# Kernel optimization log

Hardware: AMD Instinct MI355X
Metric: run time of the kernel (lower is better)

## Reference

```python
import jax, jax.numpy as jnp
import numpy as np

B, C, H, Wd = 16, 512, 56, 56
WCH = 128  # W_ch: projection rank of phi/rou


def setup_inputs() -> dict:
    key = jax.random.key(0)
    ks = jax.random.split(key, 8)
    s = 0.02
    return {
        "x": jax.random.normal(ks[0], (B, C, H, Wd), dtype=jnp.float32),
        "y": jax.random.normal(ks[1], (B, C, H, Wd), dtype=jnp.float32),
        # phi: Conv2d(C, WCH, 1) -> weight [WCH, C], bias [WCH]
        "phi_w": jax.random.normal(ks[2], (WCH, C), dtype=jnp.float32) * s,
        "phi_b": jnp.zeros((WCH,), dtype=jnp.float32),
        # rou: Conv2d(C, WCH, 1) applied to globally pooled y -> acts as Linear
        "rou_w": jax.random.normal(ks[3], (WCH, C), dtype=jnp.float32) * s,
        "rou_b": jnp.zeros((WCH,), dtype=jnp.float32),
        # zeta: Linear(C, C)
        "zeta_w": jax.random.normal(ks[4], (C, C), dtype=jnp.float32) * s,
        "zeta_b": jnp.zeros((C,), dtype=jnp.float32),
    }


def reference(x, y, phi_w, phi_b, rou_w, rou_b, zeta_w, zeta_b):
    b, c, h, w = x.shape
    hw = h * w
    # phi_xT = relu(phi(x)).view(B, WCH, HW); phi_x = transpose -> [B, HW, WCH]
    phi_xT = jax.nn.relu(jnp.einsum('kc,bchw->bkhw', phi_w, x) + phi_b[None, :, None, None])
    phi_x = phi_xT.reshape(b, -1, hw).transpose(0, 2, 1)  # [B, HW, WCH]
    # rou_y = sigmoid(rou(global_avg_pool(y))) -> [B, WCH]
    pooled = y.mean(axis=(2, 3))  # [B, C]
    rou_y = jax.nn.sigmoid(pooled @ rou_w.T + rou_b)  # [B, WCH]
    # D_i = sum_j (phi_x diag(rou) phi_x^T)_{ij} = sum_k phi_x[i,k] rou[k] s[k]
    s = phi_x.sum(axis=1)  # [B, WCH], column sums
    D = jnp.einsum('bnk,bk,bk->bn', phi_x, rou_y, s)  # [B, HW]
    inv_sqrt = 1.0 / jnp.sqrt(D + 1e-8)
    P = phi_x * inv_sqrt[..., None]  # diag(D^-1/2) @ phi_x, [B, HW, WCH]
    # x.view(B, -1, C): raw row-major reshape of [B,C,H,W] (NOT a transpose)
    x_trans = x.reshape(b, hw, c)
    # LX = x_trans - P diag(rou) P^T x_trans, re-associated right-to-left
    t = jnp.einsum('bnk,bnc->bkc', P, x_trans)          # P^T x_trans, [B, WCH, C]
    LX = x_trans - jnp.einsum('bnk,bk,bkc->bnc', P, rou_y, t)
    # zeta Linear + dropout(eval: identity) + relu, residual add
    out = jax.nn.relu(LX @ zeta_w.T + zeta_b)
    return x + out.reshape(b, c, h, w)
```

## Files before the change

kernel.cpp:

```cpp
#include <hip/hip_runtime.h>
#include <math.h>

#define B_  16
#define C_  512
#define HW_ 3136
#define K_  128
#define CHW (C_ * HW_)

typedef __bf16 bf16x8_t __attribute__((ext_vector_type(8)));
typedef __bf16 bf16x4_t __attribute__((ext_vector_type(4)));
typedef __bf16 bf16x2_t __attribute__((ext_vector_type(2)));
typedef float floatx4  __attribute__((ext_vector_type(4)));

typedef const __attribute__((address_space(1))) void* gas_ptr;
typedef __attribute__((address_space(3))) void*       las_ptr;

static __device__ __forceinline__ unsigned short bfbits(__bf16 v) {
    return __builtin_bit_cast(unsigned short, v);
}

__device__ __forceinline__ void stage128x64(const __bf16* __restrict__ base, long ld,
                                            int row0, int rowmax, int k0,
                                            __bf16* lds, int t) {
    int w = t >> 6;
    #pragma unroll
    for (int i = 0; i < 4; ++i) {
        int u = i * 256 + t;
        int m = u >> 3, slot = u & 7;
        int kg = slot ^ (m & 7);
        int r = row0 + m; if (r > rowmax) r = rowmax;
        const __bf16* g = base + (long)r * ld + (k0 + kg * 8);
        __bf16* l = lds + (size_t)(i * 256 + w * 64) * 8;
        __builtin_amdgcn_global_load_lds((gas_ptr)g, (las_ptr)l, 16, 0, 0);
    }
}

__device__ __forceinline__ void stage_tr_phi(const __bf16* __restrict__ src,
                                             int n0, int p0, char* Bs, int t) {
    int ng = t & 15;
    int cp2 = (t >> 4) * 2;
    #pragma unroll
    for (int ci = 0; ci < 2; ++ci) {
        int cc = cp2 + ci * 32;
        const __bf16* g0 = src + (long)(p0 + cc) * HW_ + n0 + ng * 8;
        bf16x8_t v0 = *(const bf16x8_t*)g0;
        bf16x8_t v1 = *(const bf16x8_t*)(g0 + HW_);
        int r8 = cc >> 3, sub = (cc & 7) >> 1;
        #pragma unroll
        for (int j = 0; j < 8; ++j) {
            int row = ng * 8 + j;
            int slot = (r8 + row + (row >> 3)) & 7;
            unsigned int pr = ((unsigned int)bfbits(v1[j]) << 16) | bfbits(v0[j]);
            *(unsigned int*)(Bs + row * 144 + slot * 16 + sub * 4) = pr;
        }
    }
}

__device__ __forceinline__ void stage_tr_t(const __bf16* __restrict__ src,
                                           const float* __restrict__ isrc,
                                           int c0, int p0, char* Bs, int t) {
    int cg = t & 15;
    int np2 = (t >> 4) * 2;
    #pragma unroll
    for (int ni = 0; ni < 2; ++ni) {
        int nn = np2 + ni * 32;
        int n = p0 + nn;
        float s0 = isrc[n], s1 = isrc[n + 1];
        const __bf16* g0 = src + (long)n * C_ + c0 + cg * 8;
        bf16x8_t v0 = *(const bf16x8_t*)g0;
        bf16x8_t v1 = *(const bf16x8_t*)(g0 + C_);
        int r8 = nn >> 3, sub = (nn & 7) >> 1;
        #pragma unroll
        for (int j = 0; j < 8; ++j) {
            int row = cg * 8 + j;
            int slot = (r8 + row + (row >> 3)) & 7;
            __bf16 a0 = (__bf16)((float)v0[j] * s0);
            __bf16 a1 = (__bf16)((float)v1[j] * s1);
            unsigned int pr = ((unsigned int)bfbits(a1) << 16) | bfbits(a0);
            *(unsigned int*)(Bs + row * 144 + slot * 16 + sub * 4) = pr;
        }
    }
}

__device__ __forceinline__ void mma_step64(const char* As, const char* Bs,
                                           floatx4 acc[4][4], int aoff, int boff,
                                           int q, int lxor) {
    #pragma unroll
    for (int h = 0; h < 2; ++h) {
        int s = (((h * 4 + q) ^ lxor) << 4);
        bf16x8_t af[4], bf[4];
        #pragma unroll
        for (int i = 0; i < 4; ++i) af[i] = *(const bf16x8_t*)(As + aoff + i * 2048 + s);
        #pragma unroll
        for (int i = 0; i < 4; ++i) bf[i] = *(const bf16x8_t*)(Bs + boff + i * 2048 + s);
        #pragma unroll
        for (int mi = 0; mi < 4; ++mi)
            #pragma unroll
            for (int ni = 0; ni < 4; ++ni)
                acc[mi][ni] = __builtin_amdgcn_mfma_f32_16x16x32_bf16(af[mi], bf[ni], acc[mi][ni], 0, 0, 0);
    }
}

__device__ __forceinline__ void mma_step_mix(const char* As, const char* Bs,
                                             floatx4 acc[4][4], int lm, int q,
                                             int wrow, int wcol) {
    int lxor = lm & 7;
    int aoff = (wrow * 64 + lm) * 128;
    #pragma unroll
    for (int h = 0; h < 2; ++h) {
        int g = h * 4 + q;
        int sa = (g ^ lxor) << 4;
        bf16x8_t af[4], bf[4];
        #pragma unroll
        for (int i = 0; i < 4; ++i) af[i] = *(const bf16x8_t*)(As + aoff + i * 2048 + sa);
        #pragma unroll
        for (int i = 0; i < 4; ++i) {
            int brow = wcol * 64 + i * 16 + lm;
            int slot = (g + brow + (brow >> 3)) & 7;
            bf[i] = *(const bf16x8_t*)(Bs + brow * 144 + slot * 16);
        }
        #pragma unroll
        for (int mi = 0; mi < 4; ++mi)
            #pragma unroll
            for (int ni = 0; ni < 4; ++ni)
                acc[mi][ni] = __builtin_amdgcn_mfma_f32_16x16x32_bf16(af[mi], bf[ni], acc[mi][ni], 0, 0, 0);
    }
}


__global__ __launch_bounds__(256) void k_pool(const float* __restrict__ y,
                                              float* __restrict__ pooled) {
    int bc = blockIdx.x;
    const float* yp = y + (long)bc * HW_;
    int t = threadIdx.x;
    float acc = 0.f;
    #pragma unroll
    for (int i = 0; i < 4; ++i) {
        int n4 = t + i * 256;
        if (n4 < 784) {
            float4 v = *reinterpret_cast<const float4*>(yp + (long)n4 * 4);
            acc += v.x + v.y + v.z + v.w;
        }
    }
    #pragma unroll
    for (int off = 32; off > 0; off >>= 1) acc += __shfl_xor(acc, off, 64);
    __shared__ float red[4];
    if ((t & 63) == 0) red[t >> 6] = acc;
    __syncthreads();
    if (t == 0) pooled[bc] = (red[0] + red[1] + red[2] + red[3]) * (1.0f / HW_);
}

__global__ __launch_bounds__(64) void k_rou(const float* __restrict__ pooled,
                                            const float* __restrict__ rou_w,
                                            const float* __restrict__ rou_b,
                                            float* __restrict__ rou_y) {
    int k = blockIdx.x;
    int b = blockIdx.y;
    int lane = threadIdx.x;
    const float* pr = pooled + b * C_;
    const float* wr = rou_w + (long)k * C_;
    float acc = 0.f;
    #pragma unroll
    for (int i = 0; i < 2; ++i) {
        int c = (lane + i * 64) * 4;
        float4 w4 = *reinterpret_cast<const float4*>(wr + c);
        float4 p4 = *reinterpret_cast<const float4*>(pr + c);
        acc += w4.x * p4.x + w4.y * p4.y + w4.z * p4.z + w4.w * p4.w;
    }
    #pragma unroll
    for (int off = 32; off > 0; off >>= 1) acc += __shfl_xor(acc, off, 64);
    if (lane == 0) rou_y[b * K_ + k] = 1.0f / (1.0f + expf(-(acc + rou_b[k])));
}

__global__ __launch_bounds__(256) void k_cast8(const float* __restrict__ a,
                                               __bf16* __restrict__ o) {
    long i = ((long)blockIdx.x * 256 + threadIdx.x) * 8;
    float4 v0 = *reinterpret_cast<const float4*>(a + i);
    float4 v1 = *reinterpret_cast<const float4*>(a + i + 4);
    bf16x8_t r;
    r[0] = (__bf16)v0.x; r[1] = (__bf16)v0.y; r[2] = (__bf16)v0.z; r[3] = (__bf16)v0.w;
    r[4] = (__bf16)v1.x; r[5] = (__bf16)v1.y; r[6] = (__bf16)v1.z; r[7] = (__bf16)v1.w;
    *reinterpret_cast<bf16x8_t*>(o + i) = r;
}


__global__ __launch_bounds__(256) void k_phi_m(const __bf16* __restrict__ xbf2,
                                               const __bf16* __restrict__ pwbf,
                                               const float* __restrict__ phi_b,
                                               __bf16* __restrict__ phi_kn,
                                               __bf16* __restrict__ phi_nk,
                                               float* __restrict__ sbuf) {
    int b = blockIdx.y;
    int n0 = blockIdx.x * 128;
    __shared__ __attribute__((aligned(16))) char smem[2 * 34816];
    int t = threadIdx.x, w = t >> 6, lane = t & 63;
    int lm = lane & 15, q = lane >> 4;
    int wrow = w >> 1, wcol = w & 1;
    floatx4 acc[4][4];
    #pragma unroll
    for (int i = 0; i < 4; ++i)
        #pragma unroll
        for (int j = 0; j < 4; ++j) acc[i][j] = (floatx4){0.f, 0.f, 0.f, 0.f};

    const __bf16* Bb = xbf2 + (long)b * CHW;

    stage128x64(pwbf, C_, 0, K_ - 1, 0, (__bf16*)smem, t);
    stage_tr_phi(Bb, n0, 0, smem + 16384, t);
    __syncthreads();
    int cur = 0;
    #pragma unroll
    for (int s = 0; s < 8; ++s) {
        char* cb = smem + cur * 34816;
        if (s < 7) {
            char* nb = smem + (cur ^ 1) * 34816;
            int p0 = (s + 1) * 64;
            stage128x64(pwbf, C_, 0, K_ - 1, p0, (__bf16*)nb, t);
            stage_tr_phi(Bb, n0, p0, nb + 16384, t);
        }
        mma_step_mix(cb, cb + 16384, acc, lm, q, wrow, wcol);
        __syncthreads();
        cur ^= 1;
    }
    #pragma unroll
    for (int mi = 0; mi < 4; ++mi) {
        int kb = wrow * 64 + mi * 16 + q * 4;
        float4 pb = *reinterpret_cast<const float4*>(phi_b + kb);
        float pbv[4] = {pb.x, pb.y, pb.z, pb.w};
        float sv[4] = {0.f, 0.f, 0.f, 0.f};
        #pragma unroll
        for (int ni = 0; ni < 4; ++ni) {
            int n = n0 + wcol * 64 + ni * 16 + lm;
            if (n < HW_) {
                bf16x4_t pack;
                #pragma unroll
                for (int r = 0; r < 4; ++r) {
                    float v = fmaxf(acc[mi][ni][r] + pbv[r], 0.f);
                    __bf16 vb = (__bf16)v;
                    phi_kn[((long)b * K_ + kb + r) * HW_ + n] = vb;
                    pack[r] = vb;
                    sv[r] += v;
                }
                *reinterpret_cast<bf16x4_t*>(phi_nk + ((long)b * HW_ + n) * K_ + kb) = pack;
            }
        }
        #pragma unroll
        for (int r = 0; r < 4; ++r) {
            float v = sv[r];
            v += __shfl_xor(v, 1, 64); v += __shfl_xor(v, 2, 64);
            v += __shfl_xor(v, 4, 64); v += __shfl_xor(v, 8, 64);
            if (lm == 0) atomicAdd(&sbuf[b * K_ + kb + r], v);
        }
    }
}

__global__ __launch_bounds__(256) void k_d2(__bf16* __restrict__ phi_nk,
                                            const float* __restrict__ rou_y,
                                            const float* __restrict__ s,
                                            float* __restrict__ inv_s) {
    int b = blockIdx.y;
    __shared__ float ws[K_];
    int t = threadIdx.x;
    if (t < K_) ws[t] = rou_y[b * K_ + t] * s[b * K_ + t];
    __syncthreads();
    int w = t >> 6, lane = t & 63;
    int n = blockIdx.x * 4 + w;
    __bf16* p = phi_nk + ((long)b * HW_ + n) * K_ + lane * 2;
    bf16x2_t v = *reinterpret_cast<bf16x2_t*>(p);
    float f0 = (float)v[0], f1 = (float)v[1];
    float d = f0 * ws[lane * 2] + f1 * ws[lane * 2 + 1];
    #pragma unroll
    for (int off = 32; off > 0; off >>= 1) d += __shfl_xor(d, off, 64);
    float inv = rsqrtf(d + 1e-8f);
    bf16x2_t o; o[0] = (__bf16)(f0 * inv); o[1] = (__bf16)(f1 * inv);
    *reinterpret_cast<bf16x2_t*>(p) = o;
    if (lane == 0) inv_s[b * HW_ + n] = inv;
}

__global__ __launch_bounds__(256) void k_t_m(const __bf16* __restrict__ phi_kn,
                                             const __bf16* __restrict__ xbf2,
                                             const float* __restrict__ inv_s,
                                             float* __restrict__ t_part) {
    int gid = blockIdx.x;
    int rlo = gid & 7, cc4 = (gid >> 3) & 3, r8 = gid >> 5;
    int r = r8 * 8 + rlo;
    int b = r / 7, nch = r % 7;
    int c0 = cc4 * 128;
    __shared__ __attribute__((aligned(16))) char smem[2 * 34816];
    int t = threadIdx.x, w = t >> 6, lane = t & 63;
    int lm = lane & 15, q = lane >> 4;
    int wrow = w >> 1, wcol = w & 1;
    floatx4 acc[4][4];
    #pragma unroll
    for (int i = 0; i < 4; ++i)
        #pragma unroll
        for (int j = 0; j < 4; ++j) acc[i][j] = (floatx4){0.f, 0.f, 0.f, 0.f};

    const __bf16* Ab = phi_kn + (long)b * K_ * HW_;
    const __bf16* Bb = xbf2 + (long)b * CHW;
    const float* ib = inv_s + (long)b * HW_;

    int pstart = nch * 448;
    stage128x64(Ab, HW_, 0, K_ - 1, pstart, (__bf16*)smem, t);
    stage_tr_t(Bb, ib, c0, pstart, smem + 16384, t);
    __syncthreads();
    int cur = 0;
    #pragma unroll
    for (int s = 0; s < 7; ++s) {
        char* cb = smem + cur * 34816;
        if (s < 6) {
            char* nb = smem + (cur ^ 1) * 34816;
            int p0 = pstart + (s + 1) * 64;
            stage128x64(Ab, HW_, 0, K_ - 1, p0, (__bf16*)nb, t);
            stage_tr_t(Bb, ib, c0, p0, nb + 16384, t);
        }
        mma_step_mix(cb, cb + 16384, acc, lm, q, wrow, wcol);
        __syncthreads();
        cur ^= 1;
    }
    float* outp = t_part + ((long)nch * B_ + b) * K_ * C_;
    #pragma unroll
    for (int mi = 0; mi < 4; ++mi) {
        int kb = wrow * 64 + mi * 16 + q * 4;
        #pragma unroll
        for (int ni = 0; ni < 4; ++ni) {
            int c = c0 + wcol * 64 + ni * 16 + lm;
            #pragma unroll
            for (int rr = 0; rr < 4; ++rr)
                outp[(long)(kb + rr) * C_ + c] = acc[mi][ni][rr];
        }
    }
}

__global__ __launch_bounds__(256) void k_tred(const float* __restrict__ t_part,
                                              __bf16* __restrict__ t_bf) {
    const long BKC = (long)B_ * K_ * C_;
    long i = ((long)blockIdx.x * 256 + threadIdx.x) * 4;
    float4 s = *reinterpret_cast<const float4*>(t_part + i);
    #pragma unroll
    for (int p = 1; p < 7; ++p) {
        float4 v = *reinterpret_cast<const float4*>(t_part + p * BKC + i);
        s.x += v.x; s.y += v.y; s.z += v.z; s.w += v.w;
    }
    bf16x4_t o;
    o[0] = (__bf16)s.x; o[1] = (__bf16)s.y; o[2] = (__bf16)s.z; o[3] = (__bf16)s.w;
    *reinterpret_cast<bf16x4_t*>(t_bf + i) = o;
}

__global__ __launch_bounds__(256) void k_tz_m(const __bf16* __restrict__ zwbf,
                                              const __bf16* __restrict__ t_bf,
                                              const float* __restrict__ rou_y,
                                              __bf16* __restrict__ tzT) {
    int b = blockIdx.y;
    int c0 = blockIdx.x * 128;
    __shared__ __attribute__((aligned(16))) char smem[2 * 32768];
    int t = threadIdx.x, w = t >> 6, lane = t & 63;
    int lm = lane & 15, q = lane >> 4;
    int wrow = w >> 1, wcol = w & 1;
    floatx4 acc[4][4];
    #pragma unroll
    for (int i = 0; i < 4; ++i)
        #pragma unroll
        for (int j = 0; j < 4; ++j) acc[i][j] = (floatx4){0.f, 0.f, 0.f, 0.f};

    const __bf16* Bb = t_bf + (long)b * K_ * C_;
    int lxor = lm & 7;
    int aoff = (wrow * 64 + lm) * 128;
    int boff = (wcol * 64 + lm) * 128;

    stage128x64(zwbf, C_, c0, C_ - 1, 0, (__bf16*)smem, t);
    stage128x64(Bb,   C_, 0, K_ - 1, 0, (__bf16*)(smem + 16384), t);
    __syncthreads();
    int cur = 0;
    #pragma unroll
    for (int s = 0; s < 8; ++s) {
        char* cb = smem + cur * 32768;
        if (s < 7) {
            char* nb = smem + (cur ^ 1) * 32768;
            int p0 = (s + 1) * 64;
            stage128x64(zwbf, C_, c0, C_ - 1, p0, (__bf16*)nb, t);
            stage128x64(Bb,   C_, 0, K_ - 1, p0, (__bf16*)(nb + 16384), t);
        }
        mma_step64(cb, cb + 16384, acc, aoff, boff, q, lxor);
        __syncthreads();
        cur ^= 1;
    }
    #pragma unroll
    for (int mi = 0; mi < 4; ++mi) {
        int c = c0 + wrow * 64 + mi * 16 + q * 4;
        #pragma unroll
        for (int ni = 0; ni < 4; ++ni) {
            int k = wcol * 64 + ni * 16 + lm;
            float rk = rou_y[b * K_ + k];
            #pragma unroll
            for (int rr = 0; rr < 4; ++rr)
                tzT[((long)b * C_ + c + rr) * K_ + k] = (__bf16)(-rk * acc[mi][ni][rr]);
        }
    }
}

__global__ __launch_bounds__(256) void k_out_m(const __bf16* __restrict__ xbf2,
                                               const __bf16* __restrict__ zwbf,
                                               const __bf16* __restrict__ pnk,
                                               const __bf16* __restrict__ tzT,
                                               const float* __restrict__ zeta_b,
                                               float* __restrict__ out) {
    int gid = blockIdx.x;
    int rlo = gid & 7, cc4 = (gid >> 3) & 3, r8 = gid >> 5;
    int r = r8 * 8 + rlo;
    int b = r / 25, nt = r % 25;
    int n0 = nt * 128;
    int c0 = cc4 * 128;
    __shared__ __attribute__((aligned(16))) char smem[2 * 32768];
    int t = threadIdx.x, w = t >> 6, lane = t & 63;
    int lm = lane & 15, q = lane >> 4;
    int wrow = w >> 1, wcol = w & 1;
    floatx4 acc[4][4];
    #pragma unroll
    for (int i = 0; i < 4; ++i)
        #pragma unroll
        for (int j = 0; j < 4; ++j) acc[i][j] = (floatx4){0.f, 0.f, 0.f, 0.f};

    int lxor = lm & 7;
    int aoff = (wrow * 64 + lm) * 128;
    int boff = (wcol * 64 + lm) * 128;

    const __bf16* A1 = xbf2 + (long)b * CHW;
    const __bf16* A2 = pnk + (long)b * (long)HW_ * K_;
    const __bf16* B2 = tzT + (long)b * (long)C_ * K_;

    stage128x64(A1,   C_, n0, HW_ - 1, 0, (__bf16*)smem, t);
    stage128x64(zwbf, C_, c0, C_ - 1, 0, (__bf16*)(smem + 16384), t);
    __syncthreads();
    int cur = 0;
    #pragma unroll
    for (int s = 0; s < 10; ++s) {
        char* cb = smem + cur * 32768;
        if (s < 9) {
            char* nb = smem + (cur ^ 1) * 32768;
            int sn = s + 1;
            if (sn < 8) {
                int p0 = sn * 64;
                stage128x64(A1,   C_, n0, HW_ - 1, p0, (__bf16*)nb, t);
                stage128x64(zwbf, C_, c0, C_ - 1, p0, (__bf16*)(nb + 16384), t);
            } else {
                int p0 = (sn - 8) * 64;
                stage128x64(A2, K_, n0, HW_ - 1, p0, (__bf16*)nb, t);
                stage128x64(B2, K_, c0, C_ - 1, p0, (__bf16*)(nb + 16384), t);
            }
        }
        mma_step64(cb, cb + 16384, acc, aoff, boff, q, lxor);
        __syncthreads();
        cur ^= 1;
    }
    float* ep = (float*)smem;
    const __bf16* xres = xbf2 + (long)b * CHW;
    int lr = t >> 3, lc = (t & 7) * 16;
    #pragma unroll
    for (int ch = 0; ch < 4; ++ch) {
        __syncthreads();
        if (wrow == (ch >> 1)) {
            #pragma unroll
            for (int mm = 0; mm < 2; ++mm) {
                int mi = (ch & 1) * 2 + mm;
                #pragma unroll
                for (int ni = 0; ni < 4; ++ni)
                    #pragma unroll
                    for (int rr = 0; rr < 4; ++rr)
                        ep[(mm * 16 + q * 4 + rr) * 132 + wcol * 64 + ni * 16 + lm] = acc[mi][ni][rr];
            }
        }
        __syncthreads();
        int n = n0 + ch * 32 + lr;
        if (n < HW_) {
            long rowbase = (long)n * C_ + c0 + lc;
            bf16x8_t x0 = *(const bf16x8_t*)(xres + rowbase);
            bf16x8_t x1 = *(const bf16x8_t*)(xres + rowbase + 8);
            float xv[16];
            #pragma unroll
            for (int j = 0; j < 8; ++j) { xv[j] = (float)x0[j]; xv[8 + j] = (float)x1[j]; }
            float* orow = out + (long)b * CHW + rowbase;
            #pragma unroll
            for (int jj = 0; jj < 4; ++jj) {
                float4 zb = *reinterpret_cast<const float4*>(zeta_b + c0 + lc + jj * 4);
                float4 e  = *reinterpret_cast<const float4*>(&ep[lr * 132 + lc + jj * 4]);
                float4 o;
                o.x = xv[jj * 4 + 0] + fmaxf(e.x + zb.x, 0.f);
                o.y = xv[jj * 4 + 1] + fmaxf(e.y + zb.y, 0.f);
                o.z = xv[jj * 4 + 2] + fmaxf(e.z + zb.z, 0.f);
                o.w = xv[jj * 4 + 3] + fmaxf(e.w + zb.w, 0.f);
                *reinterpret_cast<float4*>(orow + jj * 4) = o;
            }
        }
    }
}

extern "C" void kernel_launch(void* const* d_in, const int* in_sizes, int n_in,
                              void* d_out, int out_size, void* d_ws, size_t ws_size,
                              hipStream_t stream) {
    const float* x      = (const float*)d_in[0];
    const float* y      = (const float*)d_in[1];
    const float* phi_w  = (const float*)d_in[2];
    const float* phi_b  = (const float*)d_in[3];
    const float* rou_w  = (const float*)d_in[4];
    const float* rou_b  = (const float*)d_in[5];
    const float* zeta_w = (const float*)d_in[6];
    const float* zeta_b = (const float*)d_in[7];
    float* out = (float*)d_out;

    char* p = (char*)d_ws;
    __bf16* xbf2   = (__bf16*)p; p += (size_t)B_ * CHW * 2;
    __bf16* phi_kn = (__bf16*)p; p += (size_t)B_ * K_ * HW_ * 2;
    __bf16* phi_nk = (__bf16*)p; p += (size_t)B_ * K_ * HW_ * 2;
    float*  t_part = (float*) p; p += (size_t)7 * B_ * K_ * C_ * 4;
    __bf16* t_bf   = (__bf16*)p; p += (size_t)B_ * K_ * C_ * 2;
    __bf16* tzT    = (__bf16*)p; p += (size_t)B_ * C_ * K_ * 2;
    __bf16* pwbf   = (__bf16*)p; p += (size_t)K_ * C_ * 2;
    __bf16* zwbf   = (__bf16*)p; p += (size_t)C_ * C_ * 2;
    float*  pooled = (float*) p; p += (size_t)B_ * C_ * 4;
    float*  rou_y  = (float*) p; p += (size_t)B_ * K_ * 4;
    float*  sbuf   = (float*) p; p += (size_t)B_ * K_ * 4;
    float*  inv_s  = (float*) p; p += (size_t)B_ * HW_ * 4;

    hipMemsetAsync(sbuf, 0, B_ * K_ * sizeof(float), stream);

    k_pool <<<B_ * C_, 256, 0, stream>>>(y, pooled);
    k_rou  <<<dim3(K_, B_), 64, 0, stream>>>(pooled, rou_w, rou_b, rou_y);
    k_cast8<<<(K_ * C_) / 2048, 256, 0, stream>>>(phi_w, pwbf);
    k_cast8<<<(C_ * C_) / 2048, 256, 0, stream>>>(zeta_w, zwbf);
    k_cast8<<<(B_ * (long)CHW) / 2048, 256, 0, stream>>>(x, xbf2);
    k_phi_m<<<dim3(25, B_), 256, 0, stream>>>(xbf2, pwbf, phi_b, phi_kn, phi_nk, sbuf);
    k_d2   <<<dim3(HW_ / 4, B_), 256, 0, stream>>>(phi_nk, rou_y, sbuf, inv_s);
    k_t_m  <<<448, 256, 0, stream>>>(phi_kn, xbf2, inv_s, t_part);
    k_tred <<<(B_ * K_ * C_) / 1024, 256, 0, stream>>>(t_part, t_bf);
    k_tz_m <<<dim3(C_ / 128, B_), 256, 0, stream>>>(zwbf, t_bf, rou_y, tzT);
    k_out_m<<<1600, 256, 0, stream>>>(xbf2, zwbf, phi_nk, tzT, zeta_b, out);
}
```

Measured before the change: 389.7 us.

## Drop phi_kn copy; feed T-GEMM from normalized phi_nk via transposed staging

Removes the second (K-major) copy of phi written by k_phi_m, so phi is stored only once in [HW, K] layout. k_d2 already normalizes phi_nk in place, so k_t_m now stages both operands with a generic transposing loader and no longer rescales x by inv_sqrt during staging. This saves one bf16 phi write and reads, and moves scaling out of the inner loop. k_d2 is also widened to 8-element vector loads with four rows per wave. The cost is that the A operand in k_t_m now goes through the register transpose path, with a slightly larger LDS footprint, instead of async global-to-LDS copies.

Result: no change. 387.4 us (-0.6%).

```diff
diff --git a/kernel.cpp b/kernel.cpp
--- a/kernel.cpp
+++ b/kernel.cpp
@@ -9,7 +9,6 @@
 
 typedef __bf16 bf16x8_t __attribute__((ext_vector_type(8)));
 typedef __bf16 bf16x4_t __attribute__((ext_vector_type(4)));
-typedef __bf16 bf16x2_t __attribute__((ext_vector_type(2)));
 typedef float floatx4  __attribute__((ext_vector_type(4)));
 
 typedef const __attribute__((address_space(1))) void* gas_ptr;
@@ -35,48 +34,22 @@
     }
 }
 
-__device__ __forceinline__ void stage_tr_phi(const __bf16* __restrict__ src,
-                                             int n0, int p0, char* Bs, int t) {
-    int ng = t & 15;
-    int cp2 = (t >> 4) * 2;
+__device__ __forceinline__ void stage_tr(const __bf16* __restrict__ src, long ld,
+                                         int r0, int p0, char* Bs, int t) {
+    int rg = t & 15;
+    int pp2 = (t >> 4) * 2;
     #pragma unroll
     for (int ci = 0; ci < 2; ++ci) {
-        int cc = cp2 + ci * 32;
-        const __bf16* g0 = src + (long)(p0 + cc) * HW_ + n0 + ng * 8;
+        int cc = pp2 + ci * 32;
+        const __bf16* g0 = src + (long)(p0 + cc) * ld + r0 + rg * 8;
         bf16x8_t v0 = *(const bf16x8_t*)g0;
-        bf16x8_t v1 = *(const bf16x8_t*)(g0 + HW_);
+        bf16x8_t v1 = *(const bf16x8_t*)(g0 + ld);
         int r8 = cc >> 3, sub = (cc & 7) >> 1;
         #pragma unroll
         for (int j = 0; j < 8; ++j) {
-            int row = ng * 8 + j;
+            int row = rg * 8 + j;
             int slot = (r8 + row + (row >> 3)) & 7;
             unsigned int pr = ((unsigned int)bfbits(v1[j]) << 16) | bfbits(v0[j]);
-            *(unsigned int*)(Bs + row * 144 + slot * 16 + sub * 4) = pr;
-        }
-    }
-}
-
-__device__ __forceinline__ void stage_tr_t(const __bf16* __restrict__ src,
-                                           const float* __restrict__ isrc,
-                                           int c0, int p0, char* Bs, int t) {
-    int cg = t & 15;
-    int np2 = (t >> 4) * 2;
-    #pragma unroll
-    for (int ni = 0; ni < 2; ++ni) {
-        int nn = np2 + ni * 32;
-        int n = p0 + nn;
-        float s0 = isrc[n], s1 = isrc[n + 1];
-        const __bf16* g0 = src + (long)n * C_ + c0 + cg * 8;
-        bf16x8_t v0 = *(const bf16x8_t*)g0;
-        bf16x8_t v1 = *(const bf16x8_t*)(g0 + C_);
-        int r8 = nn >> 3, sub = (nn & 7) >> 1;
-        #pragma unroll
-        for (int j = 0; j < 8; ++j) {
-            int row = cg * 8 + j;
-            int slot = (r8 + row + (row >> 3)) & 7;
-            __bf16 a0 = (__bf16)((float)v0[j] * s0);
-            __bf16 a1 = (__bf16)((float)v1[j] * s1);
-            unsigned int pr = ((unsigned int)bfbits(a1) << 16) | bfbits(a0);
             *(unsigned int*)(Bs + row * 144 + slot * 16 + sub * 4) = pr;
         }
     }
@@ -118,6 +91,33 @@
             int brow = wcol * 64 + i * 16 + lm;
             int slot = (g + brow + (brow >> 3)) & 7;
             bf[i] = *(const bf16x8_t*)(Bs + brow * 144 + slot * 16);
+        }
+        #pragma unroll
+        for (int mi = 0; mi < 4; ++mi)
+            #pragma unroll
+            for (int ni = 0; ni < 4; ++ni)
+                acc[mi][ni] = __builtin_amdgcn_mfma_f32_16x16x32_bf16(af[mi], bf[ni], acc[mi][ni], 0, 0, 0);
+    }
+}
+
+__device__ __forceinline__ void mma_step_rot2(const char* As, const char* Bs,
+                                              floatx4 acc[4][4], int lm, int q,
+                                              int wrow, int wcol) {
+    #pragma unroll
+    for (int h = 0; h < 2; ++h) {
+        int g = h * 4 + q;
+        bf16x8_t af[4], bf[4];
+        #pragma unroll
+        for (int i = 0; i < 4; ++i) {
+            int arow = wrow * 64 + i * 16 + lm;
+            int aslot = (g + arow + (arow >> 3)) & 7;
+            af[i] = *(const bf16x8_t*)(As + arow * 144 + aslot * 16);
+        }
+        #pragma unroll
+        for (int i = 0; i < 4; ++i) {
+            int brow = wcol * 64 + i * 16 + lm;
+            int bslot = (g + brow + (brow >> 3)) & 7;
+            bf[i] = *(const bf16x8_t*)(Bs + brow * 144 + bslot * 16);
         }
         #pragma unroll
         for (int mi = 0; mi < 4; ++mi)
@@ -187,7 +187,6 @@
 __global__ __launch_bounds__(256) void k_phi_m(const __bf16* __restrict__ xbf2,
                                                const __bf16* __restrict__ pwbf,
                                                const float* __restrict__ phi_b,
-                                               __bf16* __restrict__ phi_kn,
                                                __bf16* __restrict__ phi_nk,
                                                float* __restrict__ sbuf) {
     int b = blockIdx.y;
@@ -205,7 +204,7 @@
     const __bf16* Bb = xbf2 + (long)b * CHW;
 
     stage128x64(pwbf, C_, 0, K_ - 1, 0, (__bf16*)smem, t);
-    stage_tr_phi(Bb, n0, 0, smem + 16384, t);
+    stage_tr(Bb, HW_, n0, 0, smem + 16384, t);
     __syncthreads();
     int cur = 0;
     #pragma unroll
@@ -215,7 +214,7 @@
             char* nb = smem + (cur ^ 1) * 34816;
             int p0 = (s + 1) * 64;
             stage128x64(pwbf, C_, 0, K_ - 1, p0, (__bf16*)nb, t);
-            stage_tr_phi(Bb, n0, p0, nb + 16384, t);
+            stage_tr(Bb, HW_, n0, p0, nb + 16384, t);
         }
         mma_step_mix(cb, cb + 16384, acc, lm, q, wrow, wcol);
         __syncthreads();
@@ -235,9 +234,7 @@
                 #pragma unroll
                 for (int r = 0; r < 4; ++r) {
                     float v = fmaxf(acc[mi][ni][r] + pbv[r], 0.f);
-                    __bf16 vb = (__bf16)v;
-                    phi_kn[((long)b * K_ + kb + r) * HW_ + n] = vb;
-                    pack[r] = vb;
+                    pack[r] = (__bf16)v;
                     sv[r] += v;
                 }
                 *reinterpret_cast<bf16x4_t*>(phi_nk + ((long)b * HW_ + n) * K_ + kb) = pack;
@@ -263,29 +260,35 @@
     if (t < K_) ws[t] = rou_y[b * K_ + t] * s[b * K_ + t];
     __syncthreads();
     int w = t >> 6, lane = t & 63;
-    int n = blockIdx.x * 4 + w;
-    __bf16* p = phi_nk + ((long)b * HW_ + n) * K_ + lane * 2;
-    bf16x2_t v = *reinterpret_cast<bf16x2_t*>(p);
-    float f0 = (float)v[0], f1 = (float)v[1];
-    float d = f0 * ws[lane * 2] + f1 * ws[lane * 2 + 1];
-    #pragma unroll
-    for (int off = 32; off > 0; off >>= 1) d += __shfl_xor(d, off, 64);
+    int sub = lane >> 4, lm = lane & 15;
+    int n = blockIdx.x * 16 + w * 4 + sub;
+    __bf16* p = phi_nk + ((long)b * HW_ + n) * K_ + lm * 8;
+    bf16x8_t v = *reinterpret_cast<bf16x8_t*>(p);
+    float f[8];
+    #pragma unroll
+    for (int j = 0; j < 8; ++j) f[j] = (float)v[j];
+    float d = 0.f;
+    #pragma unroll
+    for (int j = 0; j < 8; ++j) d += f[j] * ws[lm * 8 + j];
+    d += __shfl_xor(d, 1, 64); d += __shfl_xor(d, 2, 64);
+    d += __shfl_xor(d, 4, 64); d += __shfl_xor(d, 8, 64);
     float inv = rsqrtf(d + 1e-8f);
-    bf16x2_t o; o[0] = (__bf16)(f0 * inv); o[1] = (__bf16)(f1 * inv);
-    *reinterpret_cast<bf16x2_t*>(p) = o;
-    if (lane == 0) inv_s[b * HW_ + n] = inv;
-}
-
-__global__ __launch_bounds__(256) void k_t_m(const __bf16* __restrict__ phi_kn,
+    bf16x8_t o;
+    #pragma unroll
+    for (int j = 0; j < 8; ++j) o[j] = (__bf16)(f[j] * inv);
+    *reinterpret_cast<bf16x8_t*>(p) = o;
+    if (lm == 0) inv_s[b * HW_ + n] = inv;
+}
+
+__global__ __launch_bounds__(256) void k_t_m(const __bf16* __restrict__ pnk,
                                              const __bf16* __restrict__ xbf2,
-                                             const float* __restrict__ inv_s,
                                              float* __restrict__ t_part) {
     int gid = blockIdx.x;
     int rlo = gid & 7, cc4 = (gid >> 3) & 3, r8 = gid >> 5;
     int r = r8 * 8 + rlo;
     int b = r / 7, nch = r % 7;
     int c0 = cc4 * 128;
-    __shared__ __attribute__((aligned(16))) char smem[2 * 34816];
+    __shared__ __attribute__((aligned(16))) char smem[2 * 36864];
     int t = threadIdx.x, w = t >> 6, lane = t & 63;
     int lm = lane & 15, q = lane >> 4;
     int wrow = w >> 1, wcol = w & 1;
@@ -295,25 +298,24 @@
         #pragma unroll
         for (int j = 0; j < 4; ++j) acc[i][j] = (floatx4){0.f, 0.f, 0.f, 0.f};
 
-    const __bf16* Ab = phi_kn + (long)b * K_ * HW_;
+    const __bf16* Ab = pnk + (long)b * (long)HW_ * K_;
     const __bf16* Bb = xbf2 + (long)b * CHW;
-    const float* ib = inv_s + (long)b * HW_;
 
     int pstart = nch * 448;
-    stage128x64(Ab, HW_, 0, K_ - 1, pstart, (__bf16*)smem, t);
-    stage_tr_t(Bb, ib, c0, pstart, smem + 16384, t);
+    stage_tr(Ab, K_, 0, pstart, smem, t);
+    stage_tr(Bb, C_, c0, pstart, smem + 18432, t);
     __syncthreads();
     int cur = 0;
     #pragma unroll
     for (int s = 0; s < 7; ++s) {
-        char* cb = smem + cur * 34816;
+        char* cb = smem + cur * 36864;
         if (s < 6) {
-            char* nb = smem + (cur ^ 1) * 34816;
+            char* nb = smem + (cur ^ 1) * 36864;
             int p0 = pstart + (s + 1) * 64;
-            stage128x64(Ab, HW_, 0, K_ - 1, p0, (__bf16*)nb, t);
-            stage_tr_t(Bb, ib, c0, p0, nb + 16384, t);
-        }
-        mma_step_mix(cb, cb + 16384, acc, lm, q, wrow, wcol);
+            stage_tr(Ab, K_, 0, p0, nb, t);
+            stage_tr(Bb, C_, c0, p0, nb + 18432, t);
+        }
+        mma_step_rot2(cb, cb + 18432, acc, lm, q, wrow, wcol);
         __syncthreads();
         cur ^= 1;
     }
@@ -509,7 +511,6 @@
 
     char* p = (char*)d_ws;
     __bf16* xbf2   = (__bf16*)p; p += (size_t)B_ * CHW * 2;
-    __bf16* phi_kn = (__bf16*)p; p += (size_t)B_ * K_ * HW_ * 2;
     __bf16* phi_nk = (__bf16*)p; p += (size_t)B_ * K_ * HW_ * 2;
     float*  t_part = (float*) p; p += (size_t)7 * B_ * K_ * C_ * 4;
     __bf16* t_bf   = (__bf16*)p; p += (size_t)B_ * K_ * C_ * 2;
@@ -528,9 +529,9 @@
     k_cast8<<<(K_ * C_) / 2048, 256, 0, stream>>>(phi_w, pwbf);
     k_cast8<<<(C_ * C_) / 2048, 256, 0, stream>>>(zeta_w, zwbf);
     k_cast8<<<(B_ * (long)CHW) / 2048, 256, 0, stream>>>(x, xbf2);
-    k_phi_m<<<dim3(25, B_), 256, 0, stream>>>(xbf2, pwbf, phi_b, phi_kn, phi_nk, sbuf);
-    k_d2   <<<dim3(HW_ / 4, B_), 256, 0, stream>>>(phi_nk, rou_y, sbuf, inv_s);
-    k_t_m  <<<448, 256, 0, stream>>>(phi_kn, xbf2, inv_s, t_part);
+    k_phi_m<<<dim3(25, B_), 256, 0, stream>>>(xbf2, pwbf, phi_b, phi_nk, sbuf);
+    k_d2   <<<dim3(HW_ / 16, B_), 256, 0, stream>>>(phi_nk, rou_y, sbuf, inv_s);
+    k_t_m  <<<448, 256, 0, stream>>>(phi_nk, xbf2, t_part);
     k_tred <<<(B_ * K_ * C_) / 1024, 256, 0, stream>>>(t_part, t_bf);
     k_tz_m <<<dim3(C_ / 128, B_), 256, 0, stream>>>(zwbf, t_bf, rou_y, tzT);
     k_out_m<<<1600, 256, 0, stream>>>(xbf2, zwbf, phi_nk, tzT, zeta_b, out);
```
